# Kernel tuning notes

Measured on AMD Instinct MI355X. Metric: run time of the kernel, lower is better.

The kernel has to match this reference:

```python
import jax, jax.numpy as jnp
import numpy as np

N_MSB = 4
WB = 8       # weight bits
ABNM = 8     # activation bits for non-MVM ops
NL = 0.1     # noise level
B, IN, H = 256, 1024, 1024


def pact_a(x, a):
    # sign(x) * 0.5 * (|x| - ||x|-a| + a)  == sign(x)*min(|x|, a) for a>0
    return jnp.sign(x) * 0.5 * (jnp.abs(x) - jnp.abs(jnp.abs(x) - a) + a)


def _quant_val(x, bits, x_range):
    step = 2.0 ** (bits - 1)
    x01 = jnp.clip(x / x_range, -1.0 + 1.0 / step, 1.0 - 1.0 / step)
    return jnp.round(x01 * step) / step * x_range


def quant_ste(x, bits, x_range):
    # QuantFunc: straight-through estimator (identity grad wrt x, none wrt range)
    return x + jax.lax.stop_gradient(_quant_val(x, bits, x_range) - x)


def bitsplit(x, n_msb):
    # x in [0,1] -> n_msb binary planes stacked on axis 0, plus beta coefficients
    l1 = 2.0 ** n_msb - 1.0
    ys, betas = [], []
    for i in range(n_msb):
        l2 = 2.0 ** (n_msb - (i + 1))
        betas.append(l2 / l1)
        ys.append(jnp.mod(jnp.floor(jnp.round(l1 * x) / l2), 2.0))
    return jnp.stack(ys), jnp.asarray(betas, dtype=x.dtype)


def noisy_qmm(x, w, b, eps_w, eps_b):
    # CustomMM_bmm: quantized weights + gaussian noise in fwd; STE-style bwd.
    w_eff = w + jax.lax.stop_gradient(_quant_val(w, WB, 1.0) - w + eps_w * jnp.max(w) * NL)
    b_eff = b + jax.lax.stop_gradient(_quant_val(b, WB, 1.0) - b + eps_b * jnp.max(b) * NL)
    return jnp.einsum('nbi,nio->nbo', x, w_eff) + b_eff  # [n_msb, B, 4H]


def lstm_cell_q_bs(input, hx, cx, weight_ih, weight_hh, bias_ih, bias_hh,
                   eps_w_ih, eps_w_hh, eps_b_ih, eps_b_hh,
                   a1, a3, a4, a5, a6, a7, a8, a9, a10, a11):
    inp01 = (pact_a(input, a1) + a1) / (a1 * 2.0)            # [B, IN] in [0,1]
    inp_msb, beta = bitsplit(inp01, N_MSB)                   # [n_msb,B,IN], [n_msb]
    o1 = noisy_qmm(inp_msb, weight_ih, bias_ih, eps_w_ih, eps_b_ih)
    o2 = noisy_qmm(inp_msb, weight_hh, bias_hh, eps_w_hh, eps_b_hh)
    out = (o1 > 0.5).astype(inp01.dtype) + (o2 > 0.5).astype(inp01.dtype)
    gates = jnp.einsum('n,nbo->bo', beta, out)               # part1; part2 undefined in source -> 0
    i, j, f, o = jnp.split(gates, 4, axis=1)                 # each [B, H]
    forget_gate_out = quant_ste(pact_a(jax.nn.sigmoid(f), a3), ABNM, a3)
    input_gate_out = quant_ste(pact_a(jax.nn.sigmoid(i), a4), ABNM, a4)
    activation_out = quant_ste(pact_a(jnp.tanh(j), a5), ABNM, a5)
    output_gate_out = quant_ste(pact_a(jax.nn.sigmoid(o), a6), ABNM, a6)
    gated_cell = quant_ste(pact_a(cx * forget_gate_out, a7), ABNM, a7)
    activated_input = quant_ste(pact_a(input_gate_out * activation_out, a8), ABNM, a8)
    new_c = quant_ste(pact_a(gated_cell + activated_input, a9), ABNM, a9)
    activated_cell = quant_ste(pact_a(jnp.tanh(new_c), a10), ABNM, a10)
    new_h = quant_ste(pact_a(activated_cell * output_gate_out, a11), ABNM, a11)
    return new_h, new_c


def setup_inputs() -> dict:
    key = jax.random.key(0)
    ks = jax.random.split(key, 12)
    d = {
        'input': jax.random.normal(ks[0], (B, IN), jnp.float32),
        'hx': jax.random.normal(ks[1], (B, H), jnp.float32),
        'cx': jax.random.normal(ks[2], (B, H), jnp.float32),
        'weight_ih': jax.random.normal(ks[3], (N_MSB, IN, 4 * H), jnp.float32),
        'weight_hh': jax.random.normal(ks[4], (N_MSB, IN, 4 * H), jnp.float32),
        'bias_ih': jax.random.normal(ks[5], (N_MSB, 1, 4 * H), jnp.float32),
        'bias_hh': jax.random.normal(ks[6], (N_MSB, 1, 4 * H), jnp.float32),
        'eps_w_ih': jax.random.normal(ks[7], (N_MSB, IN, 4 * H), jnp.float32),
        'eps_w_hh': jax.random.normal(ks[8], (N_MSB, IN, 4 * H), jnp.float32),
        'eps_b_ih': jax.random.normal(ks[9], (N_MSB, 1, 4 * H), jnp.float32),
        'eps_b_hh': jax.random.normal(ks[10], (N_MSB, 1, 4 * H), jnp.float32),
    }
    a_init = {'a1': 128.0, 'a3': 1.0, 'a4': 1.0, 'a5': 1.0, 'a6': 1.0,
              'a7': 4.0, 'a8': 1.0, 'a9': 4.0, 'a10': 1.0, 'a11': 4.0}
    for name, v in a_init.items():
        d[name] = jnp.array([v], jnp.float32)
    return d


def reference(input, hx, cx, weight_ih, weight_hh, bias_ih, bias_hh,
              eps_w_ih, eps_w_hh, eps_b_ih, eps_b_hh,
              a1, a3, a4, a5, a6, a7, a8, a9, a10, a11):
    return lstm_cell_q_bs(input, hx, cx, weight_ih, weight_hh, bias_ih, bias_hh,
                          eps_w_ih, eps_w_hh, eps_b_ih, eps_b_hh,
                          a1, a3, a4, a5, a6, a7, a8, a9, a10, a11)
```

## Files before the change

### kernel.cpp

```cpp
#include <hip/hip_runtime.h>
#include <hip/hip_bf16.h>
#include <math.h>

typedef int   v4i __attribute__((ext_vector_type(4)));
typedef float v4f __attribute__((ext_vector_type(4)));

#define B_DIM   256
#define IN_DIM  1024
#define H4      4096
#define NPLANE  4
#define WELEM   (NPLANE * IN_DIM * H4)
#define XELEM   (B_DIM * IN_DIM)

#define WS_THRESH_OFF 64
#define WS_X_OFF      (64 + 262144)
#define WS_CMP_OFF    (64 + 262144 + 1048576)

__global__ void k_max(const float* __restrict__ wih, const float* __restrict__ whh,
                      const float* __restrict__ bih, const float* __restrict__ bhh,
                      float* __restrict__ outm) {
  int b = blockIdx.x, t = threadIdx.x;
  const float* src; long n4; int slot; long bb, nb;
  if (b < 512)       { src = wih; n4 = WELEM / 4; slot = 0; bb = b;       nb = 512; }
  else if (b < 1024) { src = whh; n4 = WELEM / 4; slot = 1; bb = b - 512; nb = 512; }
  else if (b == 1024){ src = bih; n4 = 16384 / 4; slot = 2; bb = 0;       nb = 1;   }
  else               { src = bhh; n4 = 16384 / 4; slot = 3; bb = 0;       nb = 1;   }
  const v4f* p = (const v4f*)src;
  float m = -3.4e38f;
  for (long i = bb * 256 + t; i < n4; i += nb * 256) {
    v4f v = p[i];
    m = fmaxf(m, fmaxf(fmaxf(v.x, v.y), fmaxf(v.z, v.w)));
  }
#pragma unroll
  for (int off = 32; off >= 1; off >>= 1) m = fmaxf(m, __shfl_down(m, off, 64));
  __shared__ float sm[4];
  int w = t >> 6, ln = t & 63;
  if (ln == 0) sm[w] = m;
  __syncthreads();
  if (t == 0) {
    m = fmaxf(fmaxf(sm[0], sm[1]), fmaxf(sm[2], sm[3]));
    atomicMax((int*)&outm[slot], __float_as_int(m));
  }
}

__global__ void k_prep(const float* __restrict__ input,
                       const float* __restrict__ bih, const float* __restrict__ bhh,
                       const float* __restrict__ ebih, const float* __restrict__ ebhh,
                       const float* __restrict__ a1p, const float* __restrict__ maxm,
                       double* __restrict__ thresh, signed char* __restrict__ X) {
  int gid = blockIdx.x * 256 + threadIdx.x;
  if (blockIdx.x < 1024) {
    float a1 = a1p[0];
    float x = input[gid];
    float t = fabsf(x), u = fabsf(t - a1);
    float sg = (x > 0.f) ? 0.5f : ((x < 0.f) ? -0.5f : 0.f);
    float p = sg * ((t - u) + a1);
    float inp01 = (p + a1) / (a1 * 2.0f);
    float q = rintf(15.0f * inp01);
    int qi = (int)q;
#pragma unroll
    for (int pl = 0; pl < 4; ++pl)
      X[pl * XELEM + gid] = (signed char)((qi >> (3 - pl)) & 1);
  } else {
    int i2 = gid - 262144;
    int s = i2 >> 14; int r = i2 & 16383;
    const float* bp = s ? bhh : bih;
    const float* ep = s ? ebhh : ebih;
    float mb = maxm[2 + s];
    float bv = bp[r], ev = ep[r];
    float xc = fminf(fmaxf(bv, -0.9921875f), 0.9921875f);
    float qv = rintf(xc * 128.f) * 0.0078125f;
    float noise = (ev * mb) * 0.1f;
    float beff = bv + ((qv - bv) + noise);
    thresh[i2] = 0.5 - (double)beff;
  }
}

__global__ __launch_bounds__(512, 2) void k_gemm(
    const float* __restrict__ Wih, const float* __restrict__ Whh,
    const float* __restrict__ Eih, const float* __restrict__ Ehh,
    const float* __restrict__ maxm, const double* __restrict__ thresh,
    const signed char* __restrict__ X, unsigned char* __restrict__ cmp) {
  const int ntile = blockIdx.x;
  const int sp = blockIdx.y;
  const int s = sp >> 2, plane = sp & 3;
  const float* W = s ? Whh : Wih;
  const float* E = s ? Ehh : Eih;
  const float maxw = maxm[s];

  const int tid = threadIdx.x;
  const int wave = tid >> 6, lane = tid & 63, quad = lane >> 4, l15 = lane & 15;

  __shared__ __align__(16) signed char Blds[2][4][32][80];

  v4i acc[4][2][2];
#pragma unroll
  for (int d = 0; d < 4; ++d)
#pragma unroll
    for (int m = 0; m < 2; ++m)
#pragma unroll
      for (int n = 0; n < 2; ++n) acc[d][m][n] = (v4i){0, 0, 0, 0};

  const size_t wbase = (size_t)plane * IN_DIM * H4 + (size_t)ntile * 32;
  const int kl = tid >> 3;
  const int nc4 = (tid & 7) << 2;

  const signed char* Xp = X + plane * XELEM;
  const int arow0 = wave * 32 + l15;

  auto convert_write = [&](v4f w4, v4f e4, int bf) {
#pragma unroll
    for (int e = 0; e < 4; ++e) {
      float w = w4[e], ev = e4[e];
      float xc = fminf(fmaxf(w, -0.9921875f), 0.9921875f);
      float qv = rintf(xc * 128.f) * 0.0078125f;
      float noise = (ev * maxw) * 0.1f;
      float a = w + ((qv - w) + noise);
      float x0 = a * 8.f;   float f0 = rintf(x0); float r0 = x0 - f0;
      float x1 = r0 * 128.f; float f1 = rintf(x1); float r1 = x1 - f1;
      float x2 = r1 * 128.f; float f2 = rintf(x2); float r2 = x2 - f2;
      float x3 = r2 * 128.f; float f3 = rintf(x3);
      int n = nc4 + e;
      Blds[bf][0][n][kl] = (signed char)(int)f0;
      Blds[bf][1][n][kl] = (signed char)(int)f1;
      Blds[bf][2][n][kl] = (signed char)(int)f2;
      Blds[bf][3][n][kl] = (signed char)(int)f3;
    }
  };

  {
    const float* wp = W + wbase + (size_t)kl * H4 + nc4;
    const float* ep = E + wbase + (size_t)kl * H4 + nc4;
    v4f w4 = *(const v4f*)wp;
    v4f e4 = *(const v4f*)ep;
    convert_write(w4, e4, 0);
  }
  v4i afr[2];
  afr[0] = *(const v4i*)(Xp + (arow0) * IN_DIM + quad * 16);
  afr[1] = *(const v4i*)(Xp + (arow0 + 16) * IN_DIM + quad * 16);
  __syncthreads();

  for (int ch = 0; ch < 16; ++ch) {
    const int buf = ch & 1;
    v4f w4 = {0, 0, 0, 0}, e4 = {0, 0, 0, 0};
    v4i anx[2]; anx[0] = afr[0]; anx[1] = afr[1];
    if (ch < 15) {
      const float* wp = W + wbase + (size_t)((ch + 1) * 64 + kl) * H4 + nc4;
      const float* ep = E + wbase + (size_t)((ch + 1) * 64 + kl) * H4 + nc4;
      w4 = *(const v4f*)wp;
      e4 = *(const v4f*)ep;
      anx[0] = *(const v4i*)(Xp + (arow0) * IN_DIM + (ch + 1) * 64 + quad * 16);
      anx[1] = *(const v4i*)(Xp + (arow0 + 16) * IN_DIM + (ch + 1) * 64 + quad * 16);
    }
#pragma unroll
    for (int d = 0; d < 4; ++d) {
#pragma unroll
      for (int ns = 0; ns < 2; ++ns) {
        v4i bfr = *(const v4i*)&Blds[buf][d][ns * 16 + l15][quad * 16];
        acc[d][0][ns] = __builtin_amdgcn_mfma_i32_16x16x64_i8(afr[0], bfr, acc[d][0][ns], 0, 0, 0);
        acc[d][1][ns] = __builtin_amdgcn_mfma_i32_16x16x64_i8(afr[1], bfr, acc[d][1][ns], 0, 0, 0);
      }
    }
    if (ch < 15) convert_write(w4, e4, buf ^ 1);
    afr[0] = anx[0]; afr[1] = anx[1];
    __syncthreads();
  }

  const double inv = 1.0 / 16777216.0;
  const double* thp = thresh + (size_t)sp * H4;
  unsigned char* cp = cmp + (size_t)sp * B_DIM * H4;
#pragma unroll
  for (int ms = 0; ms < 2; ++ms) {
#pragma unroll
    for (int ns = 0; ns < 2; ++ns) {
      int col = ntile * 32 + ns * 16 + l15;
      double th = thp[col];
#pragma unroll
      for (int r = 0; r < 4; ++r) {
        long long T = ((long long)acc[0][ms][ns][r] << 21) + ((long long)acc[1][ms][ns][r] << 14)
                    + ((long long)acc[2][ms][ns][r] << 7)  +  (long long)acc[3][ms][ns][r];
        int row = wave * 32 + ms * 16 + quad * 4 + r;
        cp[(size_t)row * H4 + col] = ((double)T * inv > th) ? 1 : 0;
      }
    }
  }
}

__device__ __forceinline__ float pact_(float x, float a) {
  float t = fabsf(x), u = fabsf(t - a);
  float sg = (x > 0.f) ? 0.5f : ((x < 0.f) ? -0.5f : 0.f);
  return sg * ((t - u) + a);
}
__device__ __forceinline__ float quant_(float x, float a) {
  float xr = x / a;
  xr = fminf(fmaxf(xr, -0.9921875f), 0.9921875f);
  return rintf(xr * 128.f) * 0.0078125f * a;
}
__device__ __forceinline__ float sigm_(float x) { return 1.0f / (1.0f + expf(-x)); }

__global__ void k_pointwise(const unsigned char* __restrict__ cmp, const float* __restrict__ cx,
                            const float* a3, const float* a4, const float* a5, const float* a6,
                            const float* a7, const float* a8, const float* a9, const float* a10,
                            const float* a11, float* __restrict__ out) {
  int idx = blockIdx.x * 256 + threadIdx.x;
  int b = idx >> 10, h = idx & 1023;
  float g[4];
#pragma unroll
  for (int gi = 0; gi < 4; ++gi) {
    int col = gi * 1024 + h;
    float acc = 0.f;
#pragma unroll
    for (int n = 0; n < 4; ++n) {
      int o = (int)cmp[((size_t)(0 * 4 + n) * B_DIM + b) * H4 + col]
            + (int)cmp[((size_t)(1 * 4 + n) * B_DIM + b) * H4 + col];
      float beta = (float)(8 >> n) / 15.0f;
      acc = acc + beta * (float)o;
    }
    g[gi] = acc;
  }
  float fg = quant_(pact_(sigm_(g[2]), a3[0]), a3[0]);
  float ig = quant_(pact_(sigm_(g[0]), a4[0]), a4[0]);
  float ac = quant_(pact_(tanhf(g[1]), a5[0]), a5[0]);
  float og = quant_(pact_(sigm_(g[3]), a6[0]), a6[0]);
  float cxv = cx[idx];
  float gc = quant_(pact_(cxv * fg, a7[0]), a7[0]);
  float ai = quant_(pact_(ig * ac, a8[0]), a8[0]);
  float nc = quant_(pact_(gc + ai, a9[0]), a9[0]);
  float acl = quant_(pact_(tanhf(nc), a10[0]), a10[0]);
  float nh = quant_(pact_(acl * og, a11[0]), a11[0]);
  out[idx] = nh;
  out[XELEM + idx] = nc;
}

extern "C" void kernel_launch(void* const* d_in, const int* in_sizes, int n_in,
                              void* d_out, int out_size, void* d_ws, size_t ws_size,
                              hipStream_t stream) {
  (void)in_sizes; (void)n_in; (void)out_size; (void)ws_size;
  const float* input = (const float*)d_in[0];
  const float* cx    = (const float*)d_in[2];
  const float* wih   = (const float*)d_in[3];
  const float* whh   = (const float*)d_in[4];
  const float* bih   = (const float*)d_in[5];
  const float* bhh   = (const float*)d_in[6];
  const float* ewih  = (const float*)d_in[7];
  const float* ewhh  = (const float*)d_in[8];
  const float* ebih  = (const float*)d_in[9];
  const float* ebhh  = (const float*)d_in[10];
  const float* a1    = (const float*)d_in[11];
  const float* a3    = (const float*)d_in[12];
  const float* a4    = (const float*)d_in[13];
  const float* a5    = (const float*)d_in[14];
  const float* a6    = (const float*)d_in[15];
  const float* a7    = (const float*)d_in[16];
  const float* a8    = (const float*)d_in[17];
  const float* a9    = (const float*)d_in[18];
  const float* a10   = (const float*)d_in[19];
  const float* a11   = (const float*)d_in[20];
  float* out = (float*)d_out;

  char* ws = (char*)d_ws;
  float*        maxm   = (float*)ws;
  double*       thresh = (double*)(ws + WS_THRESH_OFF);
  signed char*  X      = (signed char*)(ws + WS_X_OFF);
  unsigned char* cmp   = (unsigned char*)(ws + WS_CMP_OFF);

  hipMemsetAsync(ws, 0, 64, stream);
  k_max<<<1026, 256, 0, stream>>>(wih, whh, bih, bhh, maxm);
  k_prep<<<1152, 256, 0, stream>>>(input, bih, bhh, ebih, ebhh, a1, maxm, thresh, X);
  k_gemm<<<dim3(128, 8), 512, 0, stream>>>(wih, whh, ewih, ewhh, maxm, thresh, X, cmp);
  k_pointwise<<<1024, 256, 0, stream>>>(cmp, cx, a3, a4, a5, a6, a7, a8, a9, a10, a11, out);
}
```

Before: 334.8 us.

## Deepen GEMM prefetch pipeline, pack LDS writes, and reshape max-reduction grid

The GEMM kernel now prefetches weights, noise and activations two chunks ahead instead of one. Each thread loads four k-rows of a single column and packs the four int8 digit planes into 32-bit LDS stores, replacing byte-wise scattered stores. The block barrier becomes a custom lgkmcnt wait plus s_barrier, the chunk loop is fully unrolled, and launch bounds ask for 4 blocks per CU. The max-reduction kernel uses 4098 blocks, each doing a fixed contiguous span with an unrolled loop. The main risks are added register pressure from the deeper prefetch and the higher occupancy target, which may cause spills, and strided scalar global loads in place of float4 loads.

```diff
diff --git a/kernel.cpp b/kernel.cpp
--- a/kernel.cpp
+++ b/kernel.cpp
@@ -16,19 +16,21 @@
 #define WS_X_OFF      (64 + 262144)
 #define WS_CMP_OFF    (64 + 262144 + 1048576)
 
+#define SYNC_LDS() __asm__ volatile("s_waitcnt lgkmcnt(0)\n\ts_barrier" ::: "memory")
+
 __global__ void k_max(const float* __restrict__ wih, const float* __restrict__ whh,
                       const float* __restrict__ bih, const float* __restrict__ bhh,
                       float* __restrict__ outm) {
   int b = blockIdx.x, t = threadIdx.x;
-  const float* src; long n4; int slot; long bb, nb;
-  if (b < 512)       { src = wih; n4 = WELEM / 4; slot = 0; bb = b;       nb = 512; }
-  else if (b < 1024) { src = whh; n4 = WELEM / 4; slot = 1; bb = b - 512; nb = 512; }
-  else if (b == 1024){ src = bih; n4 = 16384 / 4; slot = 2; bb = 0;       nb = 1;   }
-  else               { src = bhh; n4 = 16384 / 4; slot = 3; bb = 0;       nb = 1;   }
-  const v4f* p = (const v4f*)src;
+  const v4f* p; int slot; size_t base; int iters;
+  if (b < 2048)      { p = (const v4f*)wih; slot = 0; base = (size_t)b * 2048;          iters = 8;  }
+  else if (b < 4096) { p = (const v4f*)whh; slot = 1; base = (size_t)(b - 2048) * 2048; iters = 8;  }
+  else if (b == 4096){ p = (const v4f*)bih; slot = 2; base = 0;                          iters = 16; }
+  else               { p = (const v4f*)bhh; slot = 3; base = 0;                          iters = 16; }
   float m = -3.4e38f;
-  for (long i = bb * 256 + t; i < n4; i += nb * 256) {
-    v4f v = p[i];
+#pragma unroll 4
+  for (int it = 0; it < iters; ++it) {
+    v4f v = p[base + (size_t)it * 256 + t];
     m = fmaxf(m, fmaxf(fmaxf(v.x, v.y), fmaxf(v.z, v.w)));
   }
 #pragma unroll
@@ -76,7 +78,7 @@
   }
 }
 
-__global__ __launch_bounds__(512, 2) void k_gemm(
+__global__ __launch_bounds__(512, 4) void k_gemm(
     const float* __restrict__ Wih, const float* __restrict__ Whh,
     const float* __restrict__ Eih, const float* __restrict__ Ehh,
     const float* __restrict__ maxm, const double* __restrict__ thresh,
@@ -101,56 +103,63 @@
 #pragma unroll
       for (int n = 0; n < 2; ++n) acc[d][m][n] = (v4i){0, 0, 0, 0};
 
-  const size_t wbase = (size_t)plane * IN_DIM * H4 + (size_t)ntile * 32;
-  const int kl = tid >> 3;
-  const int nc4 = (tid & 7) << 2;
+  const int sn  = tid & 31;
+  const int skq = tid >> 5;
+  const float* Wt = W + (size_t)plane * (IN_DIM * H4) + (size_t)(skq * 4) * H4 + ntile * 32 + sn;
+  const float* Et = E + (size_t)plane * (IN_DIM * H4) + (size_t)(skq * 4) * H4 + ntile * 32 + sn;
 
   const signed char* Xp = X + plane * XELEM;
   const int arow0 = wave * 32 + l15;
 
-  auto convert_write = [&](v4f w4, v4f e4, int bf) {
-#pragma unroll
-    for (int e = 0; e < 4; ++e) {
-      float w = w4[e], ev = e4[e];
+  auto cw = [&](const float wv[4], const float ev[4], int bf) {
+    int pk[4] = {0, 0, 0, 0};
+#pragma unroll
+    for (int j = 0; j < 4; ++j) {
+      float w = wv[j], evv = ev[j];
       float xc = fminf(fmaxf(w, -0.9921875f), 0.9921875f);
       float qv = rintf(xc * 128.f) * 0.0078125f;
-      float noise = (ev * maxw) * 0.1f;
+      float noise = (evv * maxw) * 0.1f;
       float a = w + ((qv - w) + noise);
-      float x0 = a * 8.f;   float f0 = rintf(x0); float r0 = x0 - f0;
+      float x0 = a * 8.f;    float f0 = rintf(x0); float r0 = x0 - f0;
       float x1 = r0 * 128.f; float f1 = rintf(x1); float r1 = x1 - f1;
       float x2 = r1 * 128.f; float f2 = rintf(x2); float r2 = x2 - f2;
       float x3 = r2 * 128.f; float f3 = rintf(x3);
-      int n = nc4 + e;
-      Blds[bf][0][n][kl] = (signed char)(int)f0;
-      Blds[bf][1][n][kl] = (signed char)(int)f1;
-      Blds[bf][2][n][kl] = (signed char)(int)f2;
-      Blds[bf][3][n][kl] = (signed char)(int)f3;
-    }
+      pk[0] |= ((int)f0 & 0xff) << (8 * j);
+      pk[1] |= ((int)f1 & 0xff) << (8 * j);
+      pk[2] |= ((int)f2 & 0xff) << (8 * j);
+      pk[3] |= ((int)f3 & 0xff) << (8 * j);
+    }
+#pragma unroll
+    for (int d = 0; d < 4; ++d)
+      *(int*)&Blds[bf][d][sn][skq * 4] = pk[d];
   };
 
-  {
-    const float* wp = W + wbase + (size_t)kl * H4 + nc4;
-    const float* ep = E + wbase + (size_t)kl * H4 + nc4;
-    v4f w4 = *(const v4f*)wp;
-    v4f e4 = *(const v4f*)ep;
-    convert_write(w4, e4, 0);
-  }
-  v4i afr[2];
-  afr[0] = *(const v4i*)(Xp + (arow0) * IN_DIM + quad * 16);
+  auto loadWE = [&](int ck, float wv[4], float ev[4]) {
+    size_t o = (size_t)(ck * 64) * H4;
+#pragma unroll
+    for (int j = 0; j < 4; ++j) { wv[j] = Wt[o + (size_t)j * H4]; ev[j] = Et[o + (size_t)j * H4]; }
+  };
+
+  float wA[4], eA[4], wB[4], eB[4];
+  loadWE(0, wA, eA);
+  loadWE(1, wB, eB);
+  cw(wA, eA, 0);
+  v4i afr[2], anx[2];
+  afr[0] = *(const v4i*)(Xp + (arow0)      * IN_DIM + quad * 16);
   afr[1] = *(const v4i*)(Xp + (arow0 + 16) * IN_DIM + quad * 16);
-  __syncthreads();
-
+  anx[0] = *(const v4i*)(Xp + (arow0)      * IN_DIM + 64 + quad * 16);
+  anx[1] = *(const v4i*)(Xp + (arow0 + 16) * IN_DIM + 64 + quad * 16);
+  SYNC_LDS();
+
+#pragma unroll
   for (int ch = 0; ch < 16; ++ch) {
     const int buf = ch & 1;
-    v4f w4 = {0, 0, 0, 0}, e4 = {0, 0, 0, 0};
-    v4i anx[2]; anx[0] = afr[0]; anx[1] = afr[1];
-    if (ch < 15) {
-      const float* wp = W + wbase + (size_t)((ch + 1) * 64 + kl) * H4 + nc4;
-      const float* ep = E + wbase + (size_t)((ch + 1) * 64 + kl) * H4 + nc4;
-      w4 = *(const v4f*)wp;
-      e4 = *(const v4f*)ep;
-      anx[0] = *(const v4i*)(Xp + (arow0) * IN_DIM + (ch + 1) * 64 + quad * 16);
-      anx[1] = *(const v4i*)(Xp + (arow0 + 16) * IN_DIM + (ch + 1) * 64 + quad * 16);
+    float wN[4], eN[4];
+    v4i aN[2];
+    if (ch < 14) {
+      loadWE(ch + 2, wN, eN);
+      aN[0] = *(const v4i*)(Xp + (arow0)      * IN_DIM + (ch + 2) * 64 + quad * 16);
+      aN[1] = *(const v4i*)(Xp + (arow0 + 16) * IN_DIM + (ch + 2) * 64 + quad * 16);
     }
 #pragma unroll
     for (int d = 0; d < 4; ++d) {
@@ -161,9 +170,12 @@
         acc[d][1][ns] = __builtin_amdgcn_mfma_i32_16x16x64_i8(afr[1], bfr, acc[d][1][ns], 0, 0, 0);
       }
     }
-    if (ch < 15) convert_write(w4, e4, buf ^ 1);
+    if (ch < 15) cw(wB, eB, buf ^ 1);
+#pragma unroll
+    for (int j = 0; j < 4; ++j) { wB[j] = wN[j]; eB[j] = eN[j]; }
     afr[0] = anx[0]; afr[1] = anx[1];
-    __syncthreads();
+    anx[0] = aN[0];  anx[1] = aN[1];
+    SYNC_LDS();
   }
 
   const double inv = 1.0 / 16777216.0;
@@ -259,13 +271,13 @@
   float* out = (float*)d_out;
 
   char* ws = (char*)d_ws;
-  float*        maxm   = (float*)ws;
-  double*       thresh = (double*)(ws + WS_THRESH_OFF);
-  signed char*  X      = (signed char*)(ws + WS_X_OFF);
-  unsigned char* cmp   = (unsigned char*)(ws + WS_CMP_OFF);
+  float*         maxm   = (float*)ws;
+  double*        thresh = (double*)(ws + WS_THRESH_OFF);
+  signed char*   X      = (signed char*)(ws + WS_X_OFF);
+  unsigned char* cmp    = (unsigned char*)(ws + WS_CMP_OFF);
 
   hipMemsetAsync(ws, 0, 64, stream);
-  k_max<<<1026, 256, 0, stream>>>(wih, whh, bih, bhh, maxm);
+  k_max<<<4098, 256, 0, stream>>>(wih, whh, bih, bhh, maxm);
   k_prep<<<1152, 256, 0, stream>>>(input, bih, bhh, ebih, ebhh, a1, maxm, thresh, X);
   k_gemm<<<dim3(128, 8), 512, 0, stream>>>(wih, whh, ewih, ewhh, maxm, thresh, X, cmp);
   k_pointwise<<<1024, 256, 0, stream>>>(cmp, cx, a3, a4, a5, a6, a7, a8, a9, a10, a11, out);
```

Result: slower. 346.3 us (+3.4%).
